# Kernel optimization log

Measured on AMD Instinct MI355X. Metric: run time of the kernel, lower is better.

## Reference

```python
import jax, jax.numpy as jnp
import numpy as np

ENC_VOCAB = 16000
DEC_VOCAB = 16000
HIDDEN = 1024
EMB = 512
ATTN = 512
MAX_STEPS = 512
NEG_INF = -1e30


def gru_cell(x, h, W_ih, W_hh, b_ih, b_hh):
    # torch GRU cell math. x:[B,I], h:[B,H], W_ih:[3H,I], W_hh:[3H,H]
    gi = x @ W_ih.T + b_ih
    gh = h @ W_hh.T + b_hh
    i_r, i_z, i_n = jnp.split(gi, 3, axis=1)
    h_r, h_z, h_n = jnp.split(gh, 3, axis=1)
    r = jax.nn.sigmoid(i_r + h_r)
    z = jax.nn.sigmoid(i_z + h_z)
    n = jnp.tanh(i_n + r * h_n)
    return (1.0 - z) * n + z * h


def setup_inputs() -> dict:
    key = jax.random.key(0)
    ks = jax.random.split(key, 16)
    B, T = 4, 128
    inputs = jax.random.randint(ks[0], (B, T), 0, ENC_VOCAB)

    def p(k, shape, fan_in):
        return (jax.random.normal(k, shape, dtype=jnp.float32) / np.sqrt(fan_in)).astype(jnp.float32)

    enc_emb = p(ks[1], (ENC_VOCAB, EMB), EMB)
    enc_Wih = p(ks[2], (3 * HIDDEN, EMB), EMB)
    enc_Whh = p(ks[3], (3 * HIDDEN, HIDDEN), HIDDEN)
    enc_bih = jnp.zeros((3 * HIDDEN,), jnp.float32)
    enc_bhh = jnp.zeros((3 * HIDDEN,), jnp.float32)
    dec_emb = p(ks[4], (DEC_VOCAB, EMB), EMB)
    dec_emb = dec_emb.at[0].set(0.0)  # padding_idx=0
    dec_Wih = p(ks[5], (3 * HIDDEN, EMB + ATTN), EMB + ATTN)
    dec_Whh = p(ks[6], (3 * HIDDEN, HIDDEN), HIDDEN)
    dec_bih = jnp.zeros((3 * HIDDEN,), jnp.float32)
    dec_bhh = jnp.zeros((3 * HIDDEN,), jnp.float32)
    W_av = p(ks[7], (ATTN, 2 * HIDDEN), 2 * HIDDEN)
    b_av = jnp.zeros((ATTN,), jnp.float32)
    W_cls = p(ks[8], (DEC_VOCAB, ATTN), ATTN)
    b_cls = jnp.zeros((DEC_VOCAB,), jnp.float32)
    return {
        "inputs": inputs,
        "enc_emb": enc_emb, "enc_Wih": enc_Wih, "enc_Whh": enc_Whh,
        "enc_bih": enc_bih, "enc_bhh": enc_bhh,
        "dec_emb": dec_emb, "dec_Wih": dec_Wih, "dec_Whh": dec_Whh,
        "dec_bih": dec_bih, "dec_bhh": dec_bhh,
        "W_av": W_av, "b_av": b_av, "W_cls": W_cls, "b_cls": b_cls,
    }


def seq2seq_forward(inputs, enc_emb, enc_Wih, enc_Whh, enc_bih, enc_bhh,
                    dec_emb, dec_Wih, dec_Whh, dec_bih, dec_bhh,
                    W_av, b_av, W_cls, b_cls):
    B, T = inputs.shape
    mask = inputs != 0  # [B,T]

    # ---- Encoder GRU (scan over time) ----
    emb = enc_emb[inputs]  # [B,T,E]
    h0 = jnp.zeros((B, HIDDEN), jnp.float32)

    def enc_step(h, x_t):
        h = gru_cell(x_t, h, enc_Wih, enc_Whh, enc_bih, enc_bhh)
        return h, h

    enc_ht, enc_outs = jax.lax.scan(enc_step, h0, jnp.swapaxes(emb, 0, 1))
    enc_outputs = jnp.swapaxes(enc_outs, 0, 1)  # [B,T,H]

    # ---- Decoder: 512 greedy steps ----
    ids0 = jnp.zeros((B,), jnp.int32)
    av0 = jnp.zeros((B, ATTN), jnp.float32)

    def dec_step(carry, _):
        ids, attn_vec, h = carry
        x = jnp.concatenate([dec_emb[ids], attn_vec], axis=1)  # [B,E+A]
        h = gru_cell(x, h, dec_Wih, dec_Whh, dec_bih, dec_bhh)  # [B,H]
        # attention: score = enc_outputs . h
        score = jnp.einsum('bth,bh->bt', enc_outputs, h)
        score = jnp.where(mask, score, NEG_INF)
        w = jax.nn.softmax(score, axis=1)  # [B,T]
        context = jnp.einsum('bt,bth->bh', w, enc_outputs)  # [B,H]
        merged = jnp.concatenate([context, h], axis=1)  # [B,2H]
        attn_vec = jnp.tanh(merged @ W_av.T + b_av)  # [B,A]
        logits = attn_vec @ W_cls.T + b_cls  # [B,V]
        ids = jnp.argmax(logits, axis=1).astype(jnp.int32)
        return (ids, attn_vec, h), (logits, w)

    _, (predictions, attn_weights) = jax.lax.scan(
        dec_step, (ids0, av0, enc_ht), None, length=MAX_STEPS)
    return predictions, attn_weights  # [512,B,V], [512,B,T]


def reference(inputs, enc_emb, enc_Wih, enc_Whh, enc_bih, enc_bhh,
              dec_emb, dec_Wih, dec_Whh, dec_bih, dec_bhh,
              W_av, b_av, W_cls, b_cls):
    return seq2seq_forward(inputs, enc_emb, enc_Wih, enc_Whh, enc_bih, enc_bhh,
                           dec_emb, dec_Wih, dec_Whh, dec_bih, dec_bhh,
                           W_av, b_av, W_cls, b_cls)
```

## Files before the change

kernel.cpp:

```cpp
#include <hip/hip_runtime.h>
#include <stdint.h>

typedef unsigned int u32;
typedef unsigned long long u64;

#define NBLK 256
#define NTHR 1024
#define Bz 4
#define Tz 128
#define Hz 1024
#define Ez 512
#define Az 512
#define Vz 16000
#define NSTEPS 512
#define XS 1032


__device__ __forceinline__ float sigf(float x) { return 1.0f / (1.0f + expf(-x)); }

template <int K, int L>
__device__ __forceinline__ float idot(const float4* __restrict__ w4,
                                      const float4* __restrict__ v4, int lane) {
  float4 acc = make_float4(0.f, 0.f, 0.f, 0.f);
#pragma unroll 8
  for (int k = 0; k < K; ++k) {
    float4 a = w4[lane + L * k];
    float4 b = v4[lane + L * k];
    acc.x += a.x * b.x; acc.y += a.y * b.y; acc.z += a.z * b.z; acc.w += a.w * b.w;
  }
  return (acc.x + acc.y) + (acc.z + acc.w);
}

__device__ __forceinline__ void bar_arrive(u32* ctrl, int epoch) {
  __syncthreads();
  if (threadIdx.x == 0) {
    const u32 target = (u32)epoch * 16u;
    u32* grp = ctrl + ((blockIdx.x >> 4) * 16);
    u32 v = __hip_atomic_fetch_add(grp, 1u, __ATOMIC_RELEASE, __HIP_MEMORY_SCOPE_AGENT);
    if (v == target - 1u) {
      u32 r = __hip_atomic_fetch_add(ctrl + 256, 1u, __ATOMIC_ACQ_REL, __HIP_MEMORY_SCOPE_AGENT);
      if (r == target - 1u)
        __hip_atomic_store(ctrl + 320, (u32)epoch, __ATOMIC_RELEASE, __HIP_MEMORY_SCOPE_AGENT);
    }
  }
}

__device__ __forceinline__ void bar_wait(u32* ctrl, int epoch) {
  if (threadIdx.x == 0) {
    while (__hip_atomic_load(ctrl + 320, __ATOMIC_RELAXED, __HIP_MEMORY_SCOPE_AGENT) < (u32)epoch)
      __builtin_amdgcn_s_sleep(4);
    (void)__hip_atomic_load(ctrl + 320, __ATOMIC_ACQUIRE, __HIP_MEMORY_SCOPE_AGENT);
  }
  __syncthreads();
}

__global__ void __launch_bounds__(NTHR, 1) seq2seq_kernel(
    const int* __restrict__ inputs,
    const float* __restrict__ enc_emb, const float* __restrict__ enc_Wih,
    const float* __restrict__ enc_Whh, const float* __restrict__ enc_bih,
    const float* __restrict__ enc_bhh,
    const float* __restrict__ dec_emb, const float* __restrict__ dec_Wih,
    const float* __restrict__ dec_Whh, const float* __restrict__ dec_bih,
    const float* __restrict__ dec_bhh,
    const float* __restrict__ W_av, const float* __restrict__ b_av,
    const float* __restrict__ W_cls, const float* __restrict__ b_cls,
    float* __restrict__ out, char* __restrict__ ws) {
  const int tid = threadIdx.x;
  const int bid = blockIdx.x;

  u32* ctrl = (u32*)ws;
  float* h_g = (float*)(ws + 16384);
  float* av_g = (float*)(ws + 49152);
  u64* amax_g = (u64*)(ws + 57344);
  float* encout_g = (float*)(ws + 65536);
  float* pt_g = encout_g + Bz * Tz * Hz;
  float* out_pred = out;
  float* out_aw = out + (long)NSTEPS * Bz * Vz;

  __shared__ __align__(16) float wlds[24][XS];
  __shared__ __align__(16) float x_s[Bz][XS];
  __shared__ __align__(16) float h_s[Bz][XS];
  __shared__ __align__(16) float at_s[Bz][516];
  __shared__ __align__(16) float hb_s[XS];
  __shared__ __align__(16) float e1_s[132];
  __shared__ float sc_s[128];
  __shared__ float qh_s[128];
  __shared__ float g_s[Bz][6][4];
  __shared__ float sinv_s;
  __shared__ int ids_s[Bz];
  __shared__ u64 am_s[Bz][64];

  int epoch = 0;
  const int jbase = bid * 4;
  const int t8 = tid >> 3, l8 = tid & 7;
  const int b8 = t8 / 24;
  const int r6 = t8 % 24;
  const int g6 = r6 >> 2, jl = r6 & 3;
  const int lrow = (g6 < 3) ? (g6 * 4 + jl) : (12 + (g6 - 3) * 4 + jl);
  const int grow = ((g6 < 3) ? g6 : g6 - 3) * Hz + jbase + jl;

  for (int idx = tid; idx < 12 * Ez; idx += NTHR) {
    int lr = idx >> 9, c = idx & 511;
    wlds[lr][c] = enc_Wih[(long)((lr >> 2) * Hz + jbase + (lr & 3)) * Ez + c];
  }
  for (int idx = tid; idx < 12 * Hz; idx += NTHR) {
    int lr = idx >> 10, c = idx & 1023;
    wlds[12 + lr][c] = enc_Whh[(long)((lr >> 2) * Hz + jbase + (lr & 3)) * Hz + c];
  }
  float gbias = 0.f;
  if (t8 < 96) gbias = (g6 < 3) ? enc_bih[grow] : enc_bhh[grow];
  __syncthreads();

  for (int t = 0; t < Tz; ++t) {
    float* hrd = h_g + (t & 1) * (Bz * Hz);
    float* hwr = h_g + ((t + 1) & 1) * (Bz * Hz);
    for (int idx = tid; idx < Bz * Ez; idx += NTHR) {
      int b = idx >> 9, k = idx & 511;
      x_s[b][k] = enc_emb[(long)inputs[b * Tz + t] * Ez + k];
    }
    for (int idx = tid; idx < Bz * Hz; idx += NTHR)
      h_s[idx >> 10][idx & 1023] = hrd[idx];
    __syncthreads();
    if (t8 < 96) {
      const float4* w4 = (const float4*)&wlds[lrow][0];
      float acc;
      if (g6 < 3) acc = idot<16, 8>(w4, (const float4*)&x_s[b8][0], l8);
      else        acc = idot<32, 8>(w4, (const float4*)&h_s[b8][0], l8);
      acc += __shfl_xor(acc, 1); acc += __shfl_xor(acc, 2); acc += __shfl_xor(acc, 4);
      if (l8 == 0) g_s[b8][g6][jl] = acc + gbias;
    }
    __syncthreads();
    if (tid < 16) {
      int b = tid & 3, jj = tid >> 2;
      int j = jbase + jj;
      float r = sigf(g_s[b][0][jj] + g_s[b][3][jj]);
      float z = sigf(g_s[b][1][jj] + g_s[b][4][jj]);
      float n = tanhf(g_s[b][2][jj] + r * g_s[b][5][jj]);
      float hv = (1.0f - z) * n + z * h_s[b][j];
      hwr[b * Hz + j] = hv;
      encout_g[((long)(b * Tz) + t) * Hz + j] = hv;
    }
    ++epoch; bar_arrive(ctrl, epoch); bar_wait(ctrl, epoch);
  }

  {
    int a = (bid >> 2) * 8 + (tid >> 7);
    int bt = (bid & 3) * 128 + (tid & 127);
    int b = bt >> 7, t2 = bt & 127;
    float acc = idot<256, 1>((const float4*)(W_av + (long)a * (2 * Hz)),
                             (const float4*)(encout_g + (long)bt * Hz), 0);
    pt_g[((long)(b * Az) + a) * Tz + t2] = acc;
    ++epoch; bar_arrive(ctrl, epoch); bar_wait(ctrl, epoch);
  }

  for (int idx = tid; idx < 12 * Hz; idx += NTHR) {
    int lr = idx >> 10, c = idx & 1023;
    long gr = (long)((lr >> 2) * Hz + jbase + (lr & 3));
    wlds[lr][c] = dec_Wih[gr * 1024 + c];
    wlds[12 + lr][c] = dec_Whh[gr * Hz + c];
  }
  if (t8 < 96) gbias = (g6 < 3) ? dec_bih[grow] : dec_bhh[grow];

  const int task16 = tid >> 4, l16 = tid & 15;
  const int nrows = 62 + (bid < 128 ? 1 : 0);
  const int rbase = bid * 62 + (bid < 128 ? bid : 128);
  const int myrow = rbase + (task16 < nrows ? task16 : 0);
  float4 wreg[8];
  {
    const float4* wr4 = (const float4*)(W_cls + (long)myrow * Az);
#pragma unroll
    for (int k = 0; k < 8; ++k) wreg[k] = wr4[l16 + 16 * k];
  }
  const float bclsr = b_cls[myrow];

  const int atn_b = bid & 3;
  const int abase = (bid >> 2) * 128;
  __syncthreads();

  for (int s = 0; s < NSTEPS; ++s) {
    float* hrd = h_g + (s & 1) * (Bz * Hz);
    float* hwr = h_g + ((s & 1) ^ 1) * (Bz * Hz);

    if (tid < 256) {
      int b = tid >> 6, l = tid & 63;
      u64 best = 0;
#pragma unroll
      for (int g = 0; g < 4; ++g) {
        u64 v = amax_g[(l + 64 * g) * 4 + b];
        best = v > best ? v : best;
      }
      for (int off = 32; off; off >>= 1) {
        u64 o = __shfl_xor(best, off);
        best = o > best ? o : best;
      }
      if (l == 0) ids_s[b] = (int)(0xFFFFFFFFu - (u32)(best & 0xFFFFFFFFull));
    }
    __syncthreads();
    for (int idx = tid; idx < Bz * (Ez + Az); idx += NTHR) {
      int b = idx >> 10, k = idx & 1023;
      x_s[b][k] = (k < Ez) ? dec_emb[(long)ids_s[b] * Ez + k] : av_g[b * Az + (k - Ez)];
    }
    for (int idx = tid; idx < Bz * Hz; idx += NTHR)
      h_s[idx >> 10][idx & 1023] = hrd[idx];
    __syncthreads();
    if (t8 < 96) {
      const float4* w4 = (const float4*)&wlds[lrow][0];
      const float4* v4 = (const float4*)((g6 < 3) ? &x_s[b8][0] : &h_s[b8][0]);
      float acc = idot<32, 8>(w4, v4, l8);
      acc += __shfl_xor(acc, 1); acc += __shfl_xor(acc, 2); acc += __shfl_xor(acc, 4);
      if (l8 == 0) g_s[b8][g6][jl] = acc + gbias;
    }
    __syncthreads();
    if (tid < 16) {
      int b = tid & 3, jj = tid >> 2;
      int j = jbase + jj;
      float r = sigf(g_s[b][0][jj] + g_s[b][3][jj]);
      float z = sigf(g_s[b][1][jj] + g_s[b][4][jj]);
      float n = tanhf(g_s[b][2][jj] + r * g_s[b][5][jj]);
      hwr[b * Hz + j] = (1.0f - z) * n + z * h_s[b][j];
    }
    ++epoch;
    bar_arrive(ctrl, epoch);

    if (bid < 16) {
      bar_wait(ctrl, epoch);
      const int b = atn_b;
      for (int idx = tid; idx < Hz; idx += NTHR) hb_s[idx] = hwr[b * Hz + idx];
      __syncthreads();
      {
        const int t = tid >> 3;
        float acc = idot<32, 8>((const float4*)(encout_g + ((long)(b * Tz) + t) * Hz),
                                (const float4*)hb_s, l8);
        acc += __shfl_xor(acc, 1); acc += __shfl_xor(acc, 2); acc += __shfl_xor(acc, 4);
        if (l8 == 0) sc_s[t] = (inputs[b * Tz + t] != 0) ? acc : -1e30f;
        const int a = tid >> 3;
        float qa = idot<32, 8>((const float4*)(W_av + (long)(abase + a) * (2 * Hz) + Hz),
                               (const float4*)hb_s, l8);
        qa += __shfl_xor(qa, 1); qa += __shfl_xor(qa, 2); qa += __shfl_xor(qa, 4);
        if (l8 == 0) qh_s[a] = qa;
      }
      __syncthreads();
      if (tid < 64) {
        float s0 = sc_s[tid], s1 = sc_s[64 + tid];
        float m = fmaxf(s0, s1);
#pragma unroll
        for (int off = 32; off; off >>= 1) m = fmaxf(m, __shfl_xor(m, off));
        float e0 = expf(s0 - m), e1 = expf(s1 - m);
        float sum = e0 + e1;
#pragma unroll
        for (int off = 32; off; off >>= 1) sum += __shfl_xor(sum, off);
        e1_s[tid] = e0; e1_s[64 + tid] = e1;
        if (tid == 0) sinv_s = 1.0f / sum;
      }
      __syncthreads();
      {
        const int a = tid >> 3;
        float ctx = idot<4, 8>((const float4*)(pt_g + ((long)(b * Az) + abase + a) * Tz),
                               (const float4*)e1_s, l8);
        ctx += __shfl_xor(ctx, 1); ctx += __shfl_xor(ctx, 2); ctx += __shfl_xor(ctx, 4);
        if (l8 == 0)
          av_g[b * Az + abase + a] = tanhf(ctx * sinv_s + qh_s[a] + b_av[abase + a]);
      }
      if (bid < 4 && tid < 128)
        out_aw[(long)s * (Bz * Tz) + bid * Tz + tid] = e1_s[tid] * sinv_s;
      __syncthreads();
      if (tid == 0)
        __hip_atomic_fetch_add(ctrl + 384, 1u, __ATOMIC_RELEASE, __HIP_MEMORY_SCOPE_AGENT);
    }

    if (tid == 0) {
      const u32 tgt = (u32)(16 * (s + 1));
      while (__hip_atomic_load(ctrl + 384, __ATOMIC_RELAXED, __HIP_MEMORY_SCOPE_AGENT) < tgt)
        __builtin_amdgcn_s_sleep(8);
      (void)__hip_atomic_load(ctrl + 384, __ATOMIC_ACQUIRE, __HIP_MEMORY_SCOPE_AGENT);
    }
    __syncthreads();

    for (int idx = tid; idx < Bz * Az; idx += NTHR)
      at_s[idx >> 9][idx & 511] = av_g[idx];
    __syncthreads();
#pragma unroll
    for (int b = 0; b < 4; ++b) {
      const float4* a4 = (const float4*)&at_s[b][0];
      float acc = 0.f;
#pragma unroll
      for (int k = 0; k < 8; ++k) {
        float4 a = a4[l16 + 16 * k];
        acc += wreg[k].x * a.x + wreg[k].y * a.y + wreg[k].z * a.z + wreg[k].w * a.w;
      }
      acc += __shfl_xor(acc, 1); acc += __shfl_xor(acc, 2);
      acc += __shfl_xor(acc, 4); acc += __shfl_xor(acc, 8);
      if (l16 == 0 && task16 < nrows) {
        acc += bclsr;
        out_pred[((long)s * Bz + b) * Vz + myrow] = acc;
        u32 u = __float_as_uint(acc);
        u = (u & 0x80000000u) ? ~u : (u | 0x80000000u);
        am_s[b][task16] = ((u64)u << 32) | (u64)(0xFFFFFFFFu - (u32)myrow);
      }
    }
    __syncthreads();
    if (tid < 256) {
      int b2 = tid >> 6, l = tid & 63;
      u64 best = (l < nrows) ? am_s[b2][l] : 0ull;
      for (int off = 32; off; off >>= 1) {
        u64 o = __shfl_xor(best, off);
        best = o > best ? o : best;
      }
      if (l == 0) amax_g[bid * 4 + b2] = best;
    }
    ++epoch;
    bar_arrive(ctrl, epoch);
    bar_wait(ctrl, epoch);
  }
}

extern "C" void kernel_launch(void* const* d_in, const int* in_sizes, int n_in,
                              void* d_out, int out_size, void* d_ws, size_t ws_size,
                              hipStream_t stream) {
  const int* inputs = (const int*)d_in[0];
  const float* enc_emb = (const float*)d_in[1];
  const float* enc_Wih = (const float*)d_in[2];
  const float* enc_Whh = (const float*)d_in[3];
  const float* enc_bih = (const float*)d_in[4];
  const float* enc_bhh = (const float*)d_in[5];
  const float* dec_emb = (const float*)d_in[6];
  const float* dec_Wih = (const float*)d_in[7];
  const float* dec_Whh = (const float*)d_in[8];
  const float* dec_bih = (const float*)d_in[9];
  const float* dec_bhh = (const float*)d_in[10];
  const float* W_av = (const float*)d_in[11];
  const float* b_av = (const float*)d_in[12];
  const float* W_cls = (const float*)d_in[13];
  const float* b_cls = (const float*)d_in[14];

  hipMemsetAsync(d_ws, 0, 57344, stream);
  hipMemsetAsync((char*)d_ws + 57344, 0xFF, 8192, stream);

  seq2seq_kernel<<<dim3(NBLK), dim3(NTHR), 0, stream>>>(
      inputs, enc_emb, enc_Wih, enc_Whh, enc_bih, enc_bhh,
      dec_emb, dec_Wih, dec_Whh, dec_bih, dec_bhh,
      W_av, b_av, W_cls, b_cls,
      (float*)d_out, (char*)d_ws);
}
```

Before: 19.82 ms.

## Spread decoder attention over 192 blocks with separate score and context stages

Decoder attention was handled by 16 blocks, each computing 128 scores, the query projection, softmax and 128 context outputs for one batch row. The work now goes to 64 score blocks (8 time steps each) that write scores to global memory and raise a flag, and 128 context blocks (16 attention outputs each) that compute their slice of the query projection while waiting on that flag. This shortens the serial per-step critical path by raising parallelism. In exchange it adds an extra global flag round-trip and global score traffic each step. The lrow simplification to r6 is an equivalent index rewrite.

After: 22.85 ms. 15.3% more time.

```diff
diff --git a/kernel.cpp b/kernel.cpp
--- a/kernel.cpp
+++ b/kernel.cpp
@@ -15,6 +15,9 @@
 #define NSTEPS 512
 #define XS 1032
 
+#define AVFLAG 384
+#define SCRFLAG 448
+
 
 __device__ __forceinline__ float sigf(float x) { return 1.0f / (1.0f + expf(-x)); }
 
@@ -50,6 +53,21 @@
     while (__hip_atomic_load(ctrl + 320, __ATOMIC_RELAXED, __HIP_MEMORY_SCOPE_AGENT) < (u32)epoch)
       __builtin_amdgcn_s_sleep(4);
     (void)__hip_atomic_load(ctrl + 320, __ATOMIC_ACQUIRE, __HIP_MEMORY_SCOPE_AGENT);
+  }
+  __syncthreads();
+}
+
+__device__ __forceinline__ void flag_inc(u32* ctrl, int idx) {
+  __syncthreads();
+  if (threadIdx.x == 0)
+    __hip_atomic_fetch_add(ctrl + idx, 1u, __ATOMIC_RELEASE, __HIP_MEMORY_SCOPE_AGENT);
+}
+
+__device__ __forceinline__ void flag_wait(u32* ctrl, int idx, u32 tgt) {
+  if (threadIdx.x == 0) {
+    while (__hip_atomic_load(ctrl + idx, __ATOMIC_RELAXED, __HIP_MEMORY_SCOPE_AGENT) < tgt)
+      __builtin_amdgcn_s_sleep(4);
+    (void)__hip_atomic_load(ctrl + idx, __ATOMIC_ACQUIRE, __HIP_MEMORY_SCOPE_AGENT);
   }
   __syncthreads();
 }
@@ -69,6 +87,7 @@
   const int bid = blockIdx.x;
 
   u32* ctrl = (u32*)ws;
+  float* score_g = (float*)(ws + 8192);
   float* h_g = (float*)(ws + 16384);
   float* av_g = (float*)(ws + 49152);
   u64* amax_g = (u64*)(ws + 57344);
@@ -83,8 +102,7 @@
   __shared__ __align__(16) float at_s[Bz][516];
   __shared__ __align__(16) float hb_s[XS];
   __shared__ __align__(16) float e1_s[132];
-  __shared__ float sc_s[128];
-  __shared__ float qh_s[128];
+  __shared__ float qh_s[16];
   __shared__ float g_s[Bz][6][4];
   __shared__ float sinv_s;
   __shared__ int ids_s[Bz];
@@ -96,7 +114,7 @@
   const int b8 = t8 / 24;
   const int r6 = t8 % 24;
   const int g6 = r6 >> 2, jl = r6 & 3;
-  const int lrow = (g6 < 3) ? (g6 * 4 + jl) : (12 + (g6 - 3) * 4 + jl);
+  const int lrow = r6;
   const int grow = ((g6 < 3) ? g6 : g6 - 3) * Hz + jbase + jl;
 
   for (int idx = tid; idx < 12 * Ez; idx += NTHR) {
@@ -173,8 +191,12 @@
   }
   const float bclsr = b_cls[myrow];
 
-  const int atn_b = bid & 3;
-  const int abase = (bid >> 2) * 128;
+  const bool is_ctx = bid < 128;
+  const bool is_scr = (bid >= 128) && (bid < 192);
+  const int cb = bid >> 5, ca = (bid & 31) * 16;
+  const int sgw = bid - 128;
+  const int sb = sgw >> 4, st = (sgw & 15) * 8;
+  const int wv = tid >> 6, lane = tid & 63;
   __syncthreads();
 
   for (int s = 0; s < NSTEPS; ++s) {
@@ -222,26 +244,35 @@
     ++epoch;
     bar_arrive(ctrl, epoch);
 
-    if (bid < 16) {
+    if (is_scr) {
       bar_wait(ctrl, epoch);
-      const int b = atn_b;
-      for (int idx = tid; idx < Hz; idx += NTHR) hb_s[idx] = hwr[b * Hz + idx];
+      for (int idx = tid; idx < Hz; idx += NTHR) hb_s[idx] = hwr[sb * Hz + idx];
+      __syncthreads();
+      if (wv < 8) {
+        int t = st + wv;
+        float acc = idot<4, 64>((const float4*)(encout_g + ((long)(sb * Tz) + t) * Hz),
+                                (const float4*)hb_s, lane);
+#pragma unroll
+        for (int off = 32; off; off >>= 1) acc += __shfl_xor(acc, off);
+        if (lane == 0)
+          score_g[sb * Tz + t] = (inputs[sb * Tz + t] != 0) ? acc : -1e30f;
+      }
+      flag_inc(ctrl, SCRFLAG);
+    } else if (is_ctx) {
+      bar_wait(ctrl, epoch);
+      for (int idx = tid; idx < Hz; idx += NTHR) hb_s[idx] = hwr[cb * Hz + idx];
       __syncthreads();
       {
-        const int t = tid >> 3;
-        float acc = idot<32, 8>((const float4*)(encout_g + ((long)(b * Tz) + t) * Hz),
-                                (const float4*)hb_s, l8);
-        acc += __shfl_xor(acc, 1); acc += __shfl_xor(acc, 2); acc += __shfl_xor(acc, 4);
-        if (l8 == 0) sc_s[t] = (inputs[b * Tz + t] != 0) ? acc : -1e30f;
-        const int a = tid >> 3;
-        float qa = idot<32, 8>((const float4*)(W_av + (long)(abase + a) * (2 * Hz) + Hz),
-                               (const float4*)hb_s, l8);
-        qa += __shfl_xor(qa, 1); qa += __shfl_xor(qa, 2); qa += __shfl_xor(qa, 4);
-        if (l8 == 0) qh_s[a] = qa;
-      }
-      __syncthreads();
+        int a = ca + wv;
+        float qa = idot<4, 64>((const float4*)(W_av + (long)a * (2 * Hz) + Hz),
+                               (const float4*)hb_s, lane);
+#pragma unroll
+        for (int off = 32; off; off >>= 1) qa += __shfl_xor(qa, off);
+        if (lane == 0) qh_s[wv] = qa;
+      }
+      flag_wait(ctrl, SCRFLAG, (u32)(64 * (s + 1)));
       if (tid < 64) {
-        float s0 = sc_s[tid], s1 = sc_s[64 + tid];
+        float s0 = score_g[cb * Tz + tid], s1 = score_g[cb * Tz + 64 + tid];
         float m = fmaxf(s0, s1);
 #pragma unroll
         for (int off = 32; off; off >>= 1) m = fmaxf(m, __shfl_xor(m, off));
@@ -253,28 +284,20 @@
         if (tid == 0) sinv_s = 1.0f / sum;
       }
       __syncthreads();
-      {
-        const int a = tid >> 3;
-        float ctx = idot<4, 8>((const float4*)(pt_g + ((long)(b * Az) + abase + a) * Tz),
+      if (tid < 128) {
+        int task = tid >> 3, a = ca + task;
+        float ctx = idot<4, 8>((const float4*)(pt_g + ((long)(cb * Az) + a) * Tz),
                                (const float4*)e1_s, l8);
         ctx += __shfl_xor(ctx, 1); ctx += __shfl_xor(ctx, 2); ctx += __shfl_xor(ctx, 4);
         if (l8 == 0)
-          av_g[b * Az + abase + a] = tanhf(ctx * sinv_s + qh_s[a] + b_av[abase + a]);
-      }
-      if (bid < 4 && tid < 128)
-        out_aw[(long)s * (Bz * Tz) + bid * Tz + tid] = e1_s[tid] * sinv_s;
-      __syncthreads();
-      if (tid == 0)
-        __hip_atomic_fetch_add(ctrl + 384, 1u, __ATOMIC_RELEASE, __HIP_MEMORY_SCOPE_AGENT);
-    }
-
-    if (tid == 0) {
-      const u32 tgt = (u32)(16 * (s + 1));
-      while (__hip_atomic_load(ctrl + 384, __ATOMIC_RELAXED, __HIP_MEMORY_SCOPE_AGENT) < tgt)
-        __builtin_amdgcn_s_sleep(8);
-      (void)__hip_atomic_load(ctrl + 384, __ATOMIC_ACQUIRE, __HIP_MEMORY_SCOPE_AGENT);
-    }
-    __syncthreads();
+          av_g[cb * Az + a] = tanhf(ctx * sinv_s + qh_s[task] + b_av[a]);
+      }
+      if (ca == 0 && tid < 128)
+        out_aw[(long)s * (Bz * Tz) + cb * Tz + tid] = e1_s[tid] * sinv_s;
+      flag_inc(ctrl, AVFLAG);
+    }
+
+    flag_wait(ctrl, AVFLAG, (u32)(128 * (s + 1)));
 
     for (int idx = tid; idx < Bz * Az; idx += NTHR)
       at_s[idx >> 9][idx & 511] = av_g[idx];
```

## Replace counter-based grid barriers with per-block sequence flags polled by wavefronts

Applied to the files above, without the earlier changes.

Swaps the shared atomic-counter grid barrier for per-block sequence-number arrays. Each block publishes its progress with a release store, and consumers poll all 256 (or 16) flags in parallel with one wavefront. This removes contention on a single atomic counter and lets each phase wait only on the data it depends on. It also drops one full barrier per decoder step. The risk is subtle ordering bugs, such as the h double buffer being overwritten before slow readers finish, and heavier polling traffic on the flags.

Result: slower. 20.75 ms (+4.7%).

```diff
diff --git a/kernel.cpp b/kernel.cpp
--- a/kernel.cpp
+++ b/kernel.cpp
@@ -17,6 +17,46 @@
 
 
 __device__ __forceinline__ float sigf(float x) { return 1.0f / (1.0f + expf(-x)); }
+
+__device__ __forceinline__ u32 ld_rlx(const u32* p) {
+  return __hip_atomic_load(p, __ATOMIC_RELAXED, __HIP_MEMORY_SCOPE_AGENT);
+}
+__device__ __forceinline__ void st_rel(u32* p, u32 v) {
+  __hip_atomic_store(p, v, __ATOMIC_RELEASE, __HIP_MEMORY_SCOPE_AGENT);
+}
+
+__device__ __forceinline__ void poll256(const u32* sq, u32 tgt) {
+  if (threadIdx.x < 64) {
+    const int l = threadIdx.x;
+    while (true) {
+      u32 m0 = ld_rlx(sq + l);
+      u32 m1 = ld_rlx(sq + l + 64);
+      u32 m2 = ld_rlx(sq + l + 128);
+      u32 m3 = ld_rlx(sq + l + 192);
+      u32 a = m0 < m1 ? m0 : m1;
+      u32 b = m2 < m3 ? m2 : m3;
+      u32 mn = a < b ? a : b;
+      if (__all(mn >= tgt)) break;
+      __builtin_amdgcn_s_sleep(2);
+    }
+    if (l == 0)
+      (void)__hip_atomic_load(sq, __ATOMIC_ACQUIRE, __HIP_MEMORY_SCOPE_AGENT);
+  }
+  __syncthreads();
+}
+
+__device__ __forceinline__ void poll16(const u32* sq, u32 tgt) {
+  if (threadIdx.x < 64) {
+    while (true) {
+      u32 v = (threadIdx.x < 16) ? ld_rlx(sq + threadIdx.x) : 0xFFFFFFFFu;
+      if (__all(v >= tgt)) break;
+      __builtin_amdgcn_s_sleep(2);
+    }
+    if (threadIdx.x == 0)
+      (void)__hip_atomic_load(sq, __ATOMIC_ACQUIRE, __HIP_MEMORY_SCOPE_AGENT);
+  }
+  __syncthreads();
+}
 
 template <int K, int L>
 __device__ __forceinline__ float idot(const float4* __restrict__ w4,
@@ -69,6 +109,9 @@
   const int bid = blockIdx.x;
 
   u32* ctrl = (u32*)ws;
+  u32* hseq = (u32*)(ws + 8192);
+  u32* avseq = (u32*)(ws + 9216);
+  u32* amseq = (u32*)(ws + 10240);
   float* h_g = (float*)(ws + 16384);
   float* av_g = (float*)(ws + 49152);
   u64* amax_g = (u64*)(ws + 57344);
@@ -90,13 +133,12 @@
   __shared__ int ids_s[Bz];
   __shared__ u64 am_s[Bz][64];
 
-  int epoch = 0;
   const int jbase = bid * 4;
   const int t8 = tid >> 3, l8 = tid & 7;
   const int b8 = t8 / 24;
   const int r6 = t8 % 24;
   const int g6 = r6 >> 2, jl = r6 & 3;
-  const int lrow = (g6 < 3) ? (g6 * 4 + jl) : (12 + (g6 - 3) * 4 + jl);
+  const int lrow = r6;
   const int grow = ((g6 < 3) ? g6 : g6 - 3) * Hz + jbase + jl;
 
   for (int idx = tid; idx < 12 * Ez; idx += NTHR) {
@@ -112,6 +154,7 @@
   __syncthreads();
 
   for (int t = 0; t < Tz; ++t) {
+    poll256(hseq, (u32)t);
     float* hrd = h_g + (t & 1) * (Bz * Hz);
     float* hwr = h_g + ((t + 1) & 1) * (Bz * Hz);
     for (int idx = tid; idx < Bz * Ez; idx += NTHR) {
@@ -140,9 +183,11 @@
       hwr[b * Hz + j] = hv;
       encout_g[((long)(b * Tz) + t) * Hz + j] = hv;
     }
-    ++epoch; bar_arrive(ctrl, epoch); bar_wait(ctrl, epoch);
-  }
-
+    __syncthreads();
+    if (tid == 0) st_rel(hseq + bid, (u32)(t + 1));
+  }
+
+  poll256(hseq, (u32)Tz);
   {
     int a = (bid >> 2) * 8 + (tid >> 7);
     int bt = (bid & 3) * 128 + (tid & 127);
@@ -150,8 +195,8 @@
     float acc = idot<256, 1>((const float4*)(W_av + (long)a * (2 * Hz)),
                              (const float4*)(encout_g + (long)bt * Hz), 0);
     pt_g[((long)(b * Az) + a) * Tz + t2] = acc;
-    ++epoch; bar_arrive(ctrl, epoch); bar_wait(ctrl, epoch);
-  }
+  }
+  bar_arrive(ctrl, 1); bar_wait(ctrl, 1);
 
   for (int idx = tid; idx < 12 * Hz; idx += NTHR) {
     int lr = idx >> 10, c = idx & 1023;
@@ -181,6 +226,7 @@
     float* hrd = h_g + (s & 1) * (Bz * Hz);
     float* hwr = h_g + ((s & 1) ^ 1) * (Bz * Hz);
 
+    poll256(amseq, (u32)s);
     if (tid < 256) {
       int b = tid >> 6, l = tid & 63;
       u64 best = 0;
@@ -219,11 +265,11 @@
       float n = tanhf(g_s[b][2][jj] + r * g_s[b][5][jj]);
       hwr[b * Hz + j] = (1.0f - z) * n + z * h_s[b][j];
     }
-    ++epoch;
-    bar_arrive(ctrl, epoch);
+    __syncthreads();
+    if (tid == 0) st_rel(hseq + bid, (u32)(Tz + 1 + s));
 
     if (bid < 16) {
-      bar_wait(ctrl, epoch);
+      poll256(hseq, (u32)(Tz + 1 + s));
       const int b = atn_b;
       for (int idx = tid; idx < Hz; idx += NTHR) hb_s[idx] = hwr[b * Hz + idx];
       __syncthreads();
@@ -264,17 +310,10 @@
       if (bid < 4 && tid < 128)
         out_aw[(long)s * (Bz * Tz) + bid * Tz + tid] = e1_s[tid] * sinv_s;
       __syncthreads();
-      if (tid == 0)
-        __hip_atomic_fetch_add(ctrl + 384, 1u, __ATOMIC_RELEASE, __HIP_MEMORY_SCOPE_AGENT);
-    }
-
-    if (tid == 0) {
-      const u32 tgt = (u32)(16 * (s + 1));
-      while (__hip_atomic_load(ctrl + 384, __ATOMIC_RELAXED, __HIP_MEMORY_SCOPE_AGENT) < tgt)
-        __builtin_amdgcn_s_sleep(8);
-      (void)__hip_atomic_load(ctrl + 384, __ATOMIC_ACQUIRE, __HIP_MEMORY_SCOPE_AGENT);
-    }
-    __syncthreads();
+      if (tid == 0) st_rel(avseq + bid, (u32)(s + 1));
+    }
+
+    poll16(avseq, (u32)(s + 1));
 
     for (int idx = tid; idx < Bz * Az; idx += NTHR)
       at_s[idx >> 9][idx & 511] = av_g[idx];
@@ -308,9 +347,8 @@
       }
       if (l == 0) amax_g[bid * 4 + b2] = best;
     }
-    ++epoch;
-    bar_arrive(ctrl, epoch);
-    bar_wait(ctrl, epoch);
+    __syncthreads();
+    if (tid == 0) st_rel(amseq + bid, (u32)(s + 1));
   }
 }
 
```

## Distribute decoder attention score and query dot products across all blocks as partials

Applied to the files above, without the earlier changes.

Each block keeps its 4-column slice of encoder outputs in shared memory and, right after its GRU update, computes per-block partial products for the attention scores and the W_av query term, writing them to global partial buffers. The 16 attention blocks then only reduce 256 partials per element instead of computing full 1024-long dot products from global encoder outputs. This spreads the serial attention work over all blocks. In exchange it adds an extra __syncthreads, more global writes every step, and a different floating-point summation order.

After: 25.40 ms. 28.1% more time.

```diff
diff --git a/kernel.cpp b/kernel.cpp
--- a/kernel.cpp
+++ b/kernel.cpp
@@ -27,6 +27,18 @@
     float4 a = w4[lane + L * k];
     float4 b = v4[lane + L * k];
     acc.x += a.x * b.x; acc.y += a.y * b.y; acc.z += a.z * b.z; acc.w += a.w * b.w;
+  }
+  return (acc.x + acc.y) + (acc.z + acc.w);
+}
+
+template <int K, int L>
+__device__ __forceinline__ float isum(const float* __restrict__ p, int lane) {
+  const float4* p4 = (const float4*)p;
+  float4 acc = make_float4(0.f, 0.f, 0.f, 0.f);
+#pragma unroll
+  for (int k = 0; k < K; ++k) {
+    float4 v = p4[lane + L * k];
+    acc.x += v.x; acc.y += v.y; acc.z += v.z; acc.w += v.w;
   }
   return (acc.x + acc.y) + (acc.z + acc.w);
 }
@@ -74,6 +86,8 @@
   u64* amax_g = (u64*)(ws + 57344);
   float* encout_g = (float*)(ws + 65536);
   float* pt_g = encout_g + Bz * Tz * Hz;
+  float* scorepart_g = pt_g + Bz * Az * Tz;
+  float* qhpart_g = scorepart_g + Bz * Tz * 256;
   float* out_pred = out;
   float* out_aw = out + (long)NSTEPS * Bz * Vz;
 
@@ -81,8 +95,9 @@
   __shared__ __align__(16) float x_s[Bz][XS];
   __shared__ __align__(16) float h_s[Bz][XS];
   __shared__ __align__(16) float at_s[Bz][516];
-  __shared__ __align__(16) float hb_s[XS];
   __shared__ __align__(16) float e1_s[132];
+  __shared__ __align__(16) float encpriv[Bz][Tz][4];
+  __shared__ __align__(16) float hq_s[Bz][4];
   __shared__ float sc_s[128];
   __shared__ float qh_s[128];
   __shared__ float g_s[Bz][6][4];
@@ -96,7 +111,7 @@
   const int b8 = t8 / 24;
   const int r6 = t8 % 24;
   const int g6 = r6 >> 2, jl = r6 & 3;
-  const int lrow = (g6 < 3) ? (g6 * 4 + jl) : (12 + (g6 - 3) * 4 + jl);
+  const int lrow = r6;
   const int grow = ((g6 < 3) ? g6 : g6 - 3) * Hz + jbase + jl;
 
   for (int idx = tid; idx < 12 * Ez; idx += NTHR) {
@@ -139,6 +154,7 @@
       float hv = (1.0f - z) * n + z * h_s[b][j];
       hwr[b * Hz + j] = hv;
       encout_g[((long)(b * Tz) + t) * Hz + j] = hv;
+      encpriv[b][t][jj] = hv;
     }
     ++epoch; bar_arrive(ctrl, epoch); bar_wait(ctrl, epoch);
   }
@@ -217,7 +233,26 @@
       float r = sigf(g_s[b][0][jj] + g_s[b][3][jj]);
       float z = sigf(g_s[b][1][jj] + g_s[b][4][jj]);
       float n = tanhf(g_s[b][2][jj] + r * g_s[b][5][jj]);
-      hwr[b * Hz + j] = (1.0f - z) * n + z * h_s[b][j];
+      float hv = (1.0f - z) * n + z * h_s[b][j];
+      hwr[b * Hz + j] = hv;
+      hq_s[b][jj] = hv;
+    }
+    __syncthreads();
+    if (tid < 512) {
+      int b = tid >> 7, t = tid & 127;
+      float4 e = *(const float4*)&encpriv[b][t][0];
+      float4 hq = *(const float4*)&hq_s[b][0];
+      scorepart_g[((long)(b * Tz) + t) * 256 + bid] =
+          e.x * hq.x + e.y * hq.y + e.z * hq.z + e.w * hq.w;
+    } else {
+      int a = tid - 512;
+      float4 w = *(const float4*)(W_av + (long)a * (2 * Hz) + Hz + jbase);
+#pragma unroll
+      for (int b = 0; b < 4; ++b) {
+        float4 hq = *(const float4*)&hq_s[b][0];
+        qhpart_g[((long)(b * Az) + a) * 256 + bid] =
+            w.x * hq.x + w.y * hq.y + w.z * hq.z + w.w * hq.w;
+      }
     }
     ++epoch;
     bar_arrive(ctrl, epoch);
@@ -225,17 +260,13 @@
     if (bid < 16) {
       bar_wait(ctrl, epoch);
       const int b = atn_b;
-      for (int idx = tid; idx < Hz; idx += NTHR) hb_s[idx] = hwr[b * Hz + idx];
-      __syncthreads();
       {
         const int t = tid >> 3;
-        float acc = idot<32, 8>((const float4*)(encout_g + ((long)(b * Tz) + t) * Hz),
-                                (const float4*)hb_s, l8);
+        float acc = isum<8, 8>(scorepart_g + ((long)(b * Tz) + t) * 256, l8);
         acc += __shfl_xor(acc, 1); acc += __shfl_xor(acc, 2); acc += __shfl_xor(acc, 4);
         if (l8 == 0) sc_s[t] = (inputs[b * Tz + t] != 0) ? acc : -1e30f;
         const int a = tid >> 3;
-        float qa = idot<32, 8>((const float4*)(W_av + (long)(abase + a) * (2 * Hz) + Hz),
-                               (const float4*)hb_s, l8);
+        float qa = isum<8, 8>(qhpart_g + ((long)(b * Az) + abase + a) * 256, l8);
         qa += __shfl_xor(qa, 1); qa += __shfl_xor(qa, 2); qa += __shfl_xor(qa, 4);
         if (l8 == 0) qh_s[a] = qa;
       }
```
